# Performance work log

Measured on AMD Instinct MI355X. Metric: run time of the kernel, lower is better.

The kernel has to match this reference:

```python
import jax, jax.numpy as jnp
import numpy as np

# Standard SMPL 24-joint kinematic tree (parent of joint i); parent[0] is the root.
PARENTS = np.array([0, 0, 0, 0, 1, 2, 3, 4, 5, 6, 7, 8, 9, 9, 9, 12,
                    13, 14, 16, 17, 18, 19, 20, 21], dtype=np.int64)

B, J, V = 256, 24, 6890


def setup_inputs() -> dict:
    key = jax.random.key(0)
    k1, k2, k3, k4 = jax.random.split(key, 4)
    rot_mats = jax.random.normal(k1, (B, J, 3, 3), dtype=jnp.float32)
    joints = jax.random.normal(k2, (B, J, 3), dtype=jnp.float32)
    vertices = jax.random.normal(k3, (B, V, 3), dtype=jnp.float32)
    w = jax.random.uniform(k4, (V, J), dtype=jnp.float32)
    lbs_weights = w / jnp.sum(w, axis=-1, keepdims=True)  # convex skinning weights
    return {"rot_mats": rot_mats, "joints": joints,
            "vertices": vertices, "lbs_weights": lbs_weights}


def _transform_mat(R, t):
    """R: (...,3,3), t: (...,3) -> homogeneous (...,4,4), same as torch transform_mat."""
    top = jnp.concatenate([R, t[..., None]], axis=-1)  # (...,3,4)
    bottom = jnp.broadcast_to(jnp.array([0.0, 0.0, 0.0, 1.0], dtype=R.dtype),
                              top.shape[:-2] + (1, 4))
    return jnp.concatenate([top, bottom], axis=-2)


def reference(rot_mats, joints, vertices, lbs_weights):
    # --- batch_rigid_transform ---
    # relative joint offsets w.r.t. parent
    rel_joints = joints.at[:, 1:].add(-joints[:, PARENTS[1:]])  # (B,J,3)
    T_local = _transform_mat(rot_mats, rel_joints)              # (B,J,4,4)

    # forward kinematics chain: static unroll over the fixed 24-joint tree
    chain = [T_local[:, 0]]
    for i in range(1, J):
        chain.append(chain[int(PARENTS[i])] @ T_local[:, i])
    A = jnp.stack(chain, axis=1)                                # (B,J,4,4) world transforms

    posed_joints = A[:, :, :3, 3]                               # (B,J,3)

    # rel_transforms = A - pad(A @ [j;0]) : subtract transformed rest joint from last column
    tj = jnp.einsum('bjmn,bjn->bjm', A[:, :, :, :3], joints)    # (B,J,4)
    rel_transforms = A.at[:, :, :, 3].add(-tj)                  # (B,J,4,4)

    # --- linear blend skinning ---
    T = jnp.einsum('vj,bjmn->bvmn', lbs_weights, rel_transforms)  # (B,V,4,4)
    ones = jnp.ones(vertices.shape[:-1] + (1,), dtype=vertices.dtype)
    v_h = jnp.concatenate([vertices, ones], axis=-1)              # (B,V,4)
    posed_verts = jnp.einsum('bvmn,bvn->bvm', T, v_h)[..., :3]    # (B,V,3)

    return posed_verts, posed_joints, rel_transforms
```

## Files before the change

kernel.cpp:

```cpp
#include <hip/hip_runtime.h>

#define NB 256
#define NJ 24
#define NV 6890

__global__ __launch_bounds__(32) void chain_kernel(
    const float* __restrict__ rot,
    const float* __restrict__ joints,
    float* __restrict__ posed_joints,
    float* __restrict__ rel_tf)
{
    constexpr int parents[NJ] = {0,0,0,0,1,2,3,4,5,6,7,8,9,9,9,12,13,14,16,17,18,19,20,21};
    __shared__ float Alds[NJ * 12 * 32];
    const int t = threadIdx.x;
    const int b = blockIdx.x * 32 + t;
    if (b >= NB) return;

    const float* jb = joints + (size_t)b * NJ * 3;
    const float* rb = rot + (size_t)b * NJ * 9;
    float* pj = posed_joints + (size_t)b * NJ * 3;
    float* rt = rel_tf + (size_t)b * NJ * 16;

    float jx[NJ], jy[NJ], jz[NJ];
#pragma unroll
    for (int j = 0; j < NJ; ++j) {
        jx[j] = jb[j * 3 + 0];
        jy[j] = jb[j * 3 + 1];
        jz[j] = jb[j * 3 + 2];
    }

#pragma unroll
    for (int j = 0; j < NJ; ++j) {
        float R[9];
#pragma unroll
        for (int e = 0; e < 9; ++e) R[e] = rb[j * 9 + e];

        float tx, ty, tz;
        if (j == 0) {
            tx = jx[0]; ty = jy[0]; tz = jz[0];
        } else {
            const int p = parents[j];
            tx = jx[j] - jx[p];
            ty = jy[j] - jy[p];
            tz = jz[j] - jz[p];
        }

        float A[12];
        if (j == 0) {
            A[0] = R[0]; A[1] = R[1]; A[2]  = R[2]; A[3]  = tx;
            A[4] = R[3]; A[5] = R[4]; A[6]  = R[5]; A[7]  = ty;
            A[8] = R[6]; A[9] = R[7]; A[10] = R[8]; A[11] = tz;
        } else {
            const int p = parents[j];
            float P[12];
#pragma unroll
            for (int e = 0; e < 12; ++e) P[e] = Alds[(p * 12 + e) * 32 + t];
#pragma unroll
            for (int r = 0; r < 3; ++r) {
                const float pr0 = P[r * 4 + 0], pr1 = P[r * 4 + 1];
                const float pr2 = P[r * 4 + 2], pr3 = P[r * 4 + 3];
                A[r * 4 + 0] = pr0 * R[0] + pr1 * R[3] + pr2 * R[6];
                A[r * 4 + 1] = pr0 * R[1] + pr1 * R[4] + pr2 * R[7];
                A[r * 4 + 2] = pr0 * R[2] + pr1 * R[5] + pr2 * R[8];
                A[r * 4 + 3] = pr0 * tx + pr1 * ty + pr2 * tz + pr3;
            }
        }
#pragma unroll
        for (int e = 0; e < 12; ++e) Alds[(j * 12 + e) * 32 + t] = A[e];

        pj[j * 3 + 0] = A[3];
        pj[j * 3 + 1] = A[7];
        pj[j * 3 + 2] = A[11];

        const float jjx = jx[j], jjy = jy[j], jjz = jz[j];
#pragma unroll
        for (int r = 0; r < 3; ++r) {
            rt[j * 16 + r * 4 + 0] = A[r * 4 + 0];
            rt[j * 16 + r * 4 + 1] = A[r * 4 + 1];
            rt[j * 16 + r * 4 + 2] = A[r * 4 + 2];
            rt[j * 16 + r * 4 + 3] =
                A[r * 4 + 3] - (A[r * 4 + 0] * jjx + A[r * 4 + 1] * jjy + A[r * 4 + 2] * jjz);
        }
        rt[j * 16 + 12] = 0.0f;
        rt[j * 16 + 13] = 0.0f;
        rt[j * 16 + 14] = 0.0f;
        rt[j * 16 + 15] = 1.0f;
    }
}

#define VPB 512

__global__ __launch_bounds__(256) void lbs_kernel(
    const float* __restrict__ verts,
    const float* __restrict__ weights,
    const float* __restrict__ rel_tf,
    float* __restrict__ out_verts)
{
    __shared__ float Ms[NJ * 12];
    const int tid = threadIdx.x;
    const int b = blockIdx.y;

    for (int i = tid; i < NJ * 12; i += 256) {
        const int j = i / 12;
        const int e = i % 12;
        Ms[i] = rel_tf[((size_t)b * NJ + j) * 16 + e];
    }
    __syncthreads();

    const int v0 = blockIdx.x * VPB + tid * 2;
    if (v0 >= NV) return;

    const float4* w4 = reinterpret_cast<const float4*>(weights + (size_t)v0 * NJ);
    float wreg[2 * NJ];
#pragma unroll
    for (int i = 0; i < 12; ++i) {
        const float4 q = w4[i];
        wreg[i * 4 + 0] = q.x;
        wreg[i * 4 + 1] = q.y;
        wreg[i * 4 + 2] = q.z;
        wreg[i * 4 + 3] = q.w;
    }

    const float2* vp = reinterpret_cast<const float2*>(verts + ((size_t)b * NV + v0) * 3);
    const float2 p0 = vp[0], p1 = vp[1], p2 = vp[2];
    const float x0 = p0.x, y0 = p0.y, z0 = p1.x;
    const float x1 = p1.y, y1 = p2.x, z1 = p2.y;

    float acc0[12], acc1[12];
#pragma unroll
    for (int e = 0; e < 12; ++e) { acc0[e] = 0.0f; acc1[e] = 0.0f; }

#pragma unroll
    for (int j = 0; j < NJ; ++j) {
        const float w0 = wreg[j];
        const float w1 = wreg[NJ + j];
#pragma unroll
        for (int e = 0; e < 12; ++e) {
            const float m = Ms[j * 12 + e];
            acc0[e] += w0 * m;
            acc1[e] += w1 * m;
        }
    }

    float o[6];
    o[0] = acc0[0] * x0 + acc0[1] * y0 + acc0[2]  * z0 + acc0[3];
    o[1] = acc0[4] * x0 + acc0[5] * y0 + acc0[6]  * z0 + acc0[7];
    o[2] = acc0[8] * x0 + acc0[9] * y0 + acc0[10] * z0 + acc0[11];
    o[3] = acc1[0] * x1 + acc1[1] * y1 + acc1[2]  * z1 + acc1[3];
    o[4] = acc1[4] * x1 + acc1[5] * y1 + acc1[6]  * z1 + acc1[7];
    o[5] = acc1[8] * x1 + acc1[9] * y1 + acc1[10] * z1 + acc1[11];

    float2* op = reinterpret_cast<float2*>(out_verts + ((size_t)b * NV + v0) * 3);
    op[0] = make_float2(o[0], o[1]);
    op[1] = make_float2(o[2], o[3]);
    op[2] = make_float2(o[4], o[5]);
}

extern "C" void kernel_launch(void* const* d_in, const int* in_sizes, int n_in,
                              void* d_out, int out_size, void* d_ws, size_t ws_size,
                              hipStream_t stream) {
    const float* rot     = (const float*)d_in[0];
    const float* joints  = (const float*)d_in[1];
    const float* verts   = (const float*)d_in[2];
    const float* weights = (const float*)d_in[3];

    float* out = (float*)d_out;
    float* posed_verts  = out;
    float* posed_joints = out + (size_t)NB * NV * 3;
    float* rel_tf       = posed_joints + (size_t)NB * NJ * 3;

    chain_kernel<<<dim3(NB / 32), dim3(32), 0, stream>>>(rot, joints, posed_joints, rel_tf);

    const int nblk = (NV + VPB - 1) / VPB;
    lbs_kernel<<<dim3(nblk, NB), dim3(256), 0, stream>>>(verts, weights, rel_tf, posed_verts);
}
```

Before: 123.2 us.

## Parallelize FK chain per batch, transpose weights, 4 verts per thread in LBS

Replaces the per-thread serial kinematic chain with a 288-thread block per batch that composes transforms by pointer-jumping over precomputed ancestor tables in four synchronized steps. Adds a weight transpose into workspace so the LBS kernel can load four vertices' weights per joint with one vector load. The LBS kernel now handles four vertices per thread with float4 vertex/output I/O and reads transforms straight from global memory instead of shared memory. This trades an extra kernel launch and more registers per thread for more parallel chain work and wider, coalesced memory accesses.

```diff
diff --git a/kernel.cpp b/kernel.cpp
--- a/kernel.cpp
+++ b/kernel.cpp
@@ -3,157 +3,194 @@
 #define NB 256
 #define NJ 24
 #define NV 6890
-
-__global__ __launch_bounds__(32) void chain_kernel(
+#define WT_LD 6892
+
+__global__ __launch_bounds__(256) void transpose_w(const float* __restrict__ w,
+                                                   float* __restrict__ wT) {
+    const int idx = blockIdx.x * 256 + threadIdx.x;
+    if (idx >= NV * NJ) return;
+    const int v = idx / NJ, j = idx % NJ;
+    wT[(size_t)j * WT_LD + v] = w[idx];
+}
+
+__device__ __constant__ int ANC[4][NJ] = {
+  {-1, 0, 0, 0, 1, 2, 3, 4, 5, 6, 7, 8, 9, 9, 9,12,13,14,16,17,18,19,20,21},
+  {-1,-1,-1,-1, 0, 0, 0, 1, 2, 3, 4, 5, 6, 6, 6, 9, 9, 9,13,14,16,17,18,19},
+  {-1,-1,-1,-1,-1,-1,-1,-1,-1,-1, 0, 0, 0, 0, 0, 3, 3, 3, 6, 6, 9, 9,13,14},
+  {-1,-1,-1,-1,-1,-1,-1,-1,-1,-1,-1,-1,-1,-1,-1,-1,-1,-1,-1,-1,-1,-1, 0, 0}};
+
+__global__ __launch_bounds__(288) void chain2(
     const float* __restrict__ rot,
     const float* __restrict__ joints,
     float* __restrict__ posed_joints,
     float* __restrict__ rel_tf)
 {
-    constexpr int parents[NJ] = {0,0,0,0,1,2,3,4,5,6,7,8,9,9,9,12,13,14,16,17,18,19,20,21};
-    __shared__ float Alds[NJ * 12 * 32];
-    const int t = threadIdx.x;
-    const int b = blockIdx.x * 32 + t;
-    if (b >= NB) return;
-
-    const float* jb = joints + (size_t)b * NJ * 3;
-    const float* rb = rot + (size_t)b * NJ * 9;
-    float* pj = posed_joints + (size_t)b * NJ * 3;
-    float* rt = rel_tf + (size_t)b * NJ * 16;
-
-    float jx[NJ], jy[NJ], jz[NJ];
-#pragma unroll
-    for (int j = 0; j < NJ; ++j) {
-        jx[j] = jb[j * 3 + 0];
-        jy[j] = jb[j * 3 + 1];
-        jz[j] = jb[j * 3 + 2];
-    }
-
-#pragma unroll
-    for (int j = 0; j < NJ; ++j) {
-        float R[9];
-#pragma unroll
-        for (int e = 0; e < 9; ++e) R[e] = rb[j * 9 + e];
-
-        float tx, ty, tz;
-        if (j == 0) {
-            tx = jx[0]; ty = jy[0]; tz = jz[0];
-        } else {
-            const int p = parents[j];
-            tx = jx[j] - jx[p];
-            ty = jy[j] - jy[p];
-            tz = jz[j] - jz[p];
-        }
-
-        float A[12];
-        if (j == 0) {
-            A[0] = R[0]; A[1] = R[1]; A[2]  = R[2]; A[3]  = tx;
-            A[4] = R[3]; A[5] = R[4]; A[6]  = R[5]; A[7]  = ty;
-            A[8] = R[6]; A[9] = R[7]; A[10] = R[8]; A[11] = tz;
-        } else {
-            const int p = parents[j];
-            float P[12];
-#pragma unroll
-            for (int e = 0; e < 12; ++e) P[e] = Alds[(p * 12 + e) * 32 + t];
-#pragma unroll
-            for (int r = 0; r < 3; ++r) {
-                const float pr0 = P[r * 4 + 0], pr1 = P[r * 4 + 1];
-                const float pr2 = P[r * 4 + 2], pr3 = P[r * 4 + 3];
-                A[r * 4 + 0] = pr0 * R[0] + pr1 * R[3] + pr2 * R[6];
-                A[r * 4 + 1] = pr0 * R[1] + pr1 * R[4] + pr2 * R[7];
-                A[r * 4 + 2] = pr0 * R[2] + pr1 * R[5] + pr2 * R[8];
-                A[r * 4 + 3] = pr0 * tx + pr1 * ty + pr2 * tz + pr3;
-            }
-        }
-#pragma unroll
-        for (int e = 0; e < 12; ++e) Alds[(j * 12 + e) * 32 + t] = A[e];
-
-        pj[j * 3 + 0] = A[3];
-        pj[j * 3 + 1] = A[7];
-        pj[j * 3 + 2] = A[11];
-
-        const float jjx = jx[j], jjy = jy[j], jjz = jz[j];
-#pragma unroll
-        for (int r = 0; r < 3; ++r) {
-            rt[j * 16 + r * 4 + 0] = A[r * 4 + 0];
-            rt[j * 16 + r * 4 + 1] = A[r * 4 + 1];
-            rt[j * 16 + r * 4 + 2] = A[r * 4 + 2];
-            rt[j * 16 + r * 4 + 3] =
-                A[r * 4 + 3] - (A[r * 4 + 0] * jjx + A[r * 4 + 1] * jjy + A[r * 4 + 2] * jjz);
-        }
-        rt[j * 16 + 12] = 0.0f;
-        rt[j * 16 + 13] = 0.0f;
-        rt[j * 16 + 14] = 0.0f;
-        rt[j * 16 + 15] = 1.0f;
-    }
-}
-
-#define VPB 512
-
-__global__ __launch_bounds__(256) void lbs_kernel(
+    __shared__ float Jl[NJ * 3];
+    __shared__ float MA[NJ * 12];
+    __shared__ float MB[NJ * 12];
+    const int b = blockIdx.x, tid = threadIdx.x;
+    const int j = tid / 12, e = tid % 12, r = e >> 2, c = e & 3;
+    constexpr int par[NJ] = {0,0,0,0,1,2,3,4,5,6,7,8,9,9,9,12,13,14,16,17,18,19,20,21};
+
+    if (tid < NJ * 3) Jl[tid] = joints[(size_t)b * NJ * 3 + tid];
+    __syncthreads();
+
+    float tv;
+    if (c < 3) {
+        tv = rot[(size_t)b * NJ * 9 + j * 9 + r * 3 + c];
+    } else {
+        tv = Jl[j * 3 + r];
+        if (j > 0) tv -= Jl[par[j] * 3 + r];
+    }
+    MA[j * 12 + e] = tv;
+    __syncthreads();
+
+#define DSTEP(SRC, DST, K)                                                 \
+    do {                                                                   \
+        const int a = ANC[K][j];                                           \
+        float nv;                                                          \
+        if (a < 0) {                                                       \
+            nv = SRC[j * 12 + e];                                          \
+        } else {                                                           \
+            nv = SRC[a * 12 + r * 4 + 0] * SRC[j * 12 + 0 + c]            \
+               + SRC[a * 12 + r * 4 + 1] * SRC[j * 12 + 4 + c]            \
+               + SRC[a * 12 + r * 4 + 2] * SRC[j * 12 + 8 + c];           \
+            if (c == 3) nv += SRC[a * 12 + r * 4 + 3];                    \
+        }                                                                  \
+        DST[j * 12 + e] = nv;                                              \
+        __syncthreads();                                                   \
+    } while (0)
+
+    DSTEP(MA, MB, 0);
+    DSTEP(MB, MA, 1);
+    DSTEP(MA, MB, 2);
+    DSTEP(MB, MA, 3);
+
+    const float aje = MA[j * 12 + e];
+    if (c == 3) {
+        posed_joints[(size_t)b * NJ * 3 + j * 3 + r] = aje;
+        const float tj = MA[j * 12 + r * 4 + 0] * Jl[j * 3 + 0]
+                       + MA[j * 12 + r * 4 + 1] * Jl[j * 3 + 1]
+                       + MA[j * 12 + r * 4 + 2] * Jl[j * 3 + 2];
+        rel_tf[(size_t)b * NJ * 16 + j * 16 + e] = aje - tj;
+    } else {
+        rel_tf[(size_t)b * NJ * 16 + j * 16 + e] = aje;
+    }
+    if (tid < NJ * 4) {
+        const int j2 = tid >> 2, c2 = tid & 3;
+        rel_tf[(size_t)b * NJ * 16 + j2 * 16 + 12 + c2] = (c2 == 3) ? 1.0f : 0.0f;
+    }
+}
+
+__device__ __forceinline__ float f4c(const float4& q, int l) {
+    switch (l) {
+        case 0: return q.x;
+        case 1: return q.y;
+        case 2: return q.z;
+        default: return q.w;
+    }
+}
+
+template <bool WT>
+__global__ __launch_bounds__(256) void lbs2(
     const float* __restrict__ verts,
-    const float* __restrict__ weights,
+    const float* __restrict__ wgt,
+    const float* __restrict__ wTp,
     const float* __restrict__ rel_tf,
     float* __restrict__ out_verts)
 {
-    __shared__ float Ms[NJ * 12];
-    const int tid = threadIdx.x;
-    const int b = blockIdx.y;
-
-    for (int i = tid; i < NJ * 12; i += 256) {
-        const int j = i / 12;
-        const int e = i % 12;
-        Ms[i] = rel_tf[((size_t)b * NJ + j) * 16 + e];
-    }
-    __syncthreads();
-
-    const int v0 = blockIdx.x * VPB + tid * 2;
+    const int b = blockIdx.y, tid = threadIdx.x;
+    const int v0 = blockIdx.x * 1024 + tid * 4;
     if (v0 >= NV) return;
-
-    const float4* w4 = reinterpret_cast<const float4*>(weights + (size_t)v0 * NJ);
-    float wreg[2 * NJ];
-#pragma unroll
-    for (int i = 0; i < 12; ++i) {
-        const float4 q = w4[i];
-        wreg[i * 4 + 0] = q.x;
-        wreg[i * 4 + 1] = q.y;
-        wreg[i * 4 + 2] = q.z;
-        wreg[i * 4 + 3] = q.w;
-    }
-
-    const float2* vp = reinterpret_cast<const float2*>(verts + ((size_t)b * NV + v0) * 3);
-    const float2 p0 = vp[0], p1 = vp[1], p2 = vp[2];
-    const float x0 = p0.x, y0 = p0.y, z0 = p1.x;
-    const float x1 = p1.y, y1 = p2.x, z1 = p2.y;
-
-    float acc0[12], acc1[12];
-#pragma unroll
-    for (int e = 0; e < 12; ++e) { acc0[e] = 0.0f; acc1[e] = 0.0f; }
-
-#pragma unroll
-    for (int j = 0; j < NJ; ++j) {
-        const float w0 = wreg[j];
-        const float w1 = wreg[NJ + j];
-#pragma unroll
-        for (int e = 0; e < 12; ++e) {
-            const float m = Ms[j * 12 + e];
-            acc0[e] += w0 * m;
-            acc1[e] += w1 * m;
+    const float* __restrict__ Mb = rel_tf + (size_t)b * NJ * 16;
+
+    float acc[4][12];
+#pragma unroll
+    for (int v = 0; v < 4; ++v)
+#pragma unroll
+        for (int q = 0; q < 12; ++q) acc[v][q] = 0.0f;
+
+    if (v0 + 4 <= NV) {
+        if (WT) {
+#pragma unroll
+            for (int jj = 0; jj < NJ; ++jj) {
+                const float4 wv = *reinterpret_cast<const float4*>(wTp + (size_t)jj * WT_LD + v0);
+                const float4 m0 = *reinterpret_cast<const float4*>(Mb + jj * 16 + 0);
+                const float4 m1 = *reinterpret_cast<const float4*>(Mb + jj * 16 + 4);
+                const float4 m2 = *reinterpret_cast<const float4*>(Mb + jj * 16 + 8);
+                const float m[12] = {m0.x, m0.y, m0.z, m0.w, m1.x, m1.y,
+                                     m1.z, m1.w, m2.x, m2.y, m2.z, m2.w};
+                const float wl[4] = {wv.x, wv.y, wv.z, wv.w};
+#pragma unroll
+                for (int v = 0; v < 4; ++v)
+#pragma unroll
+                    for (int q = 0; q < 12; ++q) acc[v][q] += wl[v] * m[q];
+            }
+        } else {
+#pragma unroll
+            for (int jc = 0; jc < 6; ++jc) {
+                float4 wq[4];
+#pragma unroll
+                for (int v = 0; v < 4; ++v)
+                    wq[v] = *reinterpret_cast<const float4*>(wgt + (size_t)(v0 + v) * NJ + jc * 4);
+#pragma unroll
+                for (int l = 0; l < 4; ++l) {
+                    const int jj = jc * 4 + l;
+                    const float4 m0 = *reinterpret_cast<const float4*>(Mb + jj * 16 + 0);
+                    const float4 m1 = *reinterpret_cast<const float4*>(Mb + jj * 16 + 4);
+                    const float4 m2 = *reinterpret_cast<const float4*>(Mb + jj * 16 + 8);
+                    const float m[12] = {m0.x, m0.y, m0.z, m0.w, m1.x, m1.y,
+                                         m1.z, m1.w, m2.x, m2.y, m2.z, m2.w};
+                    const float wl[4] = {f4c(wq[0], l), f4c(wq[1], l), f4c(wq[2], l), f4c(wq[3], l)};
+#pragma unroll
+                    for (int v = 0; v < 4; ++v)
+#pragma unroll
+                        for (int q = 0; q < 12; ++q) acc[v][q] += wl[v] * m[q];
+                }
+            }
         }
-    }
-
-    float o[6];
-    o[0] = acc0[0] * x0 + acc0[1] * y0 + acc0[2]  * z0 + acc0[3];
-    o[1] = acc0[4] * x0 + acc0[5] * y0 + acc0[6]  * z0 + acc0[7];
-    o[2] = acc0[8] * x0 + acc0[9] * y0 + acc0[10] * z0 + acc0[11];
-    o[3] = acc1[0] * x1 + acc1[1] * y1 + acc1[2]  * z1 + acc1[3];
-    o[4] = acc1[4] * x1 + acc1[5] * y1 + acc1[6]  * z1 + acc1[7];
-    o[5] = acc1[8] * x1 + acc1[9] * y1 + acc1[10] * z1 + acc1[11];
-
-    float2* op = reinterpret_cast<float2*>(out_verts + ((size_t)b * NV + v0) * 3);
-    op[0] = make_float2(o[0], o[1]);
-    op[1] = make_float2(o[2], o[3]);
-    op[2] = make_float2(o[4], o[5]);
+
+        const float* vp = verts + ((size_t)b * NV + v0) * 3;
+        const float4 p0 = *reinterpret_cast<const float4*>(vp + 0);
+        const float4 p1 = *reinterpret_cast<const float4*>(vp + 4);
+        const float4 p2 = *reinterpret_cast<const float4*>(vp + 8);
+        const float px[4] = {p0.x, p0.w, p1.z, p2.y};
+        const float py[4] = {p0.y, p1.x, p1.w, p2.z};
+        const float pz[4] = {p0.z, p1.y, p2.x, p2.w};
+
+        float o[12];
+#pragma unroll
+        for (int v = 0; v < 4; ++v)
+#pragma unroll
+            for (int rr = 0; rr < 3; ++rr)
+                o[v * 3 + rr] = acc[v][rr * 4 + 0] * px[v] + acc[v][rr * 4 + 1] * py[v] +
+                                acc[v][rr * 4 + 2] * pz[v] + acc[v][rr * 4 + 3];
+
+        float* op = out_verts + ((size_t)b * NV + v0) * 3;
+        *reinterpret_cast<float4*>(op + 0) = make_float4(o[0], o[1], o[2],  o[3]);
+        *reinterpret_cast<float4*>(op + 4) = make_float4(o[4], o[5], o[6],  o[7]);
+        *reinterpret_cast<float4*>(op + 8) = make_float4(o[8], o[9], o[10], o[11]);
+    } else {
+        for (int vi = 0; vi < 4; ++vi) {
+            const int v = v0 + vi;
+            if (v >= NV) break;
+            float a[12];
+#pragma unroll
+            for (int q = 0; q < 12; ++q) a[q] = 0.0f;
+#pragma unroll
+            for (int jj = 0; jj < NJ; ++jj) {
+                const float wv = WT ? wTp[(size_t)jj * WT_LD + v] : wgt[(size_t)v * NJ + jj];
+#pragma unroll
+                for (int q = 0; q < 12; ++q) a[q] += wv * Mb[jj * 16 + q];
+            }
+            const float* vp = verts + ((size_t)b * NV + v) * 3;
+            const float x = vp[0], y = vp[1], z = vp[2];
+            float* op = out_verts + ((size_t)b * NV + v) * 3;
+            op[0] = a[0] * x + a[1] * y + a[2]  * z + a[3];
+            op[1] = a[4] * x + a[5] * y + a[6]  * z + a[7];
+            op[2] = a[8] * x + a[9] * y + a[10] * z + a[11];
+        }
+    }
 }
 
 extern "C" void kernel_launch(void* const* d_in, const int* in_sizes, int n_in,
@@ -169,8 +206,20 @@
     float* posed_joints = out + (size_t)NB * NV * 3;
     float* rel_tf       = posed_joints + (size_t)NB * NJ * 3;
 
-    chain_kernel<<<dim3(NB / 32), dim3(32), 0, stream>>>(rot, joints, posed_joints, rel_tf);
-
-    const int nblk = (NV + VPB - 1) / VPB;
-    lbs_kernel<<<dim3(nblk, NB), dim3(256), 0, stream>>>(verts, weights, rel_tf, posed_verts);
-}
+    const size_t WT_BYTES = (size_t)NJ * WT_LD * sizeof(float);
+    const bool use_wt = (d_ws != nullptr) && (ws_size >= WT_BYTES);
+
+    if (use_wt) {
+        transpose_w<<<(NV * NJ + 255) / 256, 256, 0, stream>>>(weights, (float*)d_ws);
+    }
+    chain2<<<NB, 288, 0, stream>>>(rot, joints, posed_joints, rel_tf);
+
+    const int nbx = (NV + 1023) / 1024;
+    if (use_wt) {
+        lbs2<true><<<dim3(nbx, NB), 256, 0, stream>>>(verts, weights, (const float*)d_ws,
+                                                      rel_tf, posed_verts);
+    } else {
+        lbs2<false><<<dim3(nbx, NB), 256, 0, stream>>>(verts, weights, nullptr,
+                                                       rel_tf, posed_verts);
+    }
+}
```

Result: slower. 128.8 us (+4.6%).
